# Performance work log

Hardware: AMD Instinct MI355X
Metric: run time of the kernel (lower is better)

The kernel has to match this reference:

```python
import jax, jax.numpy as jnp
import numpy as np
import math

B, N, L = 1, 256, 384
D_MSA, D_PAIR, H, DH = 256, 128, 8, 32
EPS = 1e-5


def layernorm(x, g, b):
    mu = jnp.mean(x, axis=-1, keepdims=True)
    var = jnp.mean(jnp.square(x - mu), axis=-1, keepdims=True)
    return (x - mu) * jax.lax.rsqrt(var + EPS) * g + b


def setup_inputs() -> dict:
    key = jax.random.key(0)
    ks = jax.random.split(key, 16)
    s_msa = 1.0 / math.sqrt(D_MSA)
    s_pair = 1.0 / math.sqrt(D_PAIR)
    s_hd = 1.0 / math.sqrt(H * DH)
    return {
        "msa": jax.random.normal(ks[0], (B, N, L, D_MSA), jnp.float32),
        "pair": jax.random.normal(ks[1], (B, L, L, D_PAIR), jnp.float32),
        "ln_msa_g": jnp.ones((D_MSA,), jnp.float32),
        "ln_msa_b": jnp.zeros((D_MSA,), jnp.float32),
        "ln_pair_g": jnp.ones((D_PAIR,), jnp.float32),
        "ln_pair_b": jnp.zeros((D_PAIR,), jnp.float32),
        # SequenceWeight projections (stored as (in, out): y = x @ W + b)
        "Wq_sw": jax.random.normal(ks[2], (D_MSA, H * DH), jnp.float32) * s_msa,
        "bq_sw": jnp.zeros((H * DH,), jnp.float32),
        "Wk_sw": jax.random.normal(ks[3], (D_MSA, H * DH), jnp.float32) * s_msa,
        "bk_sw": jnp.zeros((H * DH,), jnp.float32),
        # Main attention projections (bias-free q/k/v)
        "Wq": jax.random.normal(ks[4], (D_MSA, H * DH), jnp.float32) * s_msa,
        "Wk": jax.random.normal(ks[5], (D_MSA, H * DH), jnp.float32) * s_msa,
        "Wv": jax.random.normal(ks[6], (D_MSA, H * DH), jnp.float32) * s_msa,
        "Wb": jax.random.normal(ks[7], (D_PAIR, H), jnp.float32) * s_pair,
        "Wg": jax.random.normal(ks[8], (D_MSA, H * DH), jnp.float32) * s_msa,
        "bg": jnp.ones((H * DH,), jnp.float32),
        "Wo": jax.random.normal(ks[9], (H * DH, D_MSA), jnp.float32) * s_hd,
        "bo": jnp.zeros((D_MSA,), jnp.float32),
    }


def reference(msa, pair, ln_msa_g, ln_msa_b, ln_pair_g, ln_pair_b,
              Wq_sw, bq_sw, Wk_sw, bk_sw, Wq, Wk, Wv, Wb, Wg, bg, Wo, bo):
    b, n, l, _ = msa.shape
    scale = 1.0 / math.sqrt(DH)

    m = layernorm(msa, ln_msa_g, ln_msa_b)  # (B,N,L,d_msa)

    # --- SequenceWeight: per-sequence, per-position, per-head weights ---
    q_sw = (m[:, 0] @ Wq_sw + bq_sw).reshape(b, l, H, DH) * scale   # (B,L,h,d)
    k_sw = (m @ Wk_sw + bk_sw).reshape(b, n, l, H, DH)              # (B,N,L,h,d)
    sw_logits = jnp.einsum('bihd,bnihd->bnih', q_sw, k_sw)
    seq_weight = jax.nn.softmax(sw_logits, axis=1)[..., None]       # (B,N,L,h,1)

    # --- Row attention with pair bias ---
    q = (m @ Wq).reshape(b, n, l, H, DH) * seq_weight               # seq-weighted queries
    k = (m @ Wk).reshape(b, n, l, H, DH) * scale
    logits = jnp.einsum('bnihd,bnjhd->bijh', q, k)                  # sum over N and d
    bias = layernorm(pair, ln_pair_g, ln_pair_b) @ Wb               # (B,L,L,h)
    attn = jax.nn.softmax(logits + bias, axis=2)                    # softmax over j

    v = (m @ Wv).reshape(b, n, l, H, DH)
    out = jnp.einsum('bijh,bnjhd->bnihd', attn, v).reshape(b, n, l, H * DH)

    gate = jax.nn.sigmoid(m @ Wg + bg)
    return (out * gate) @ Wo + bo                                   # (B,N,L,d_msa)
```

## Files before the change

kernel.cpp:

```cpp
#include <hip/hip_runtime.h>
#include <stdint.h>

#define NSEQ 256
#define LRES 384
#define NH   8
#define NL   (NSEQ*LRES)
#define SCALE 0.17677669529663687f

typedef unsigned short u16;
typedef unsigned int   u32;
typedef short bf16x8 __attribute__((ext_vector_type(8)));
typedef float f32x4  __attribute__((ext_vector_type(4)));

__device__ __forceinline__ u16 f2bf(float f) {
    u32 x = __float_as_uint(f);
    return (u16)((x + 0x7fffu + ((x >> 16) & 1u)) >> 16);
}
__device__ __forceinline__ u32 pack2(float a, float b) {
    u32 xa = __float_as_uint(a);
    u32 xb = __float_as_uint(b);
    xa = (xa + 0x7fffu + ((xa >> 16) & 1u)) >> 16;
    xb = ((xb + 0x7fffu + ((xb >> 16) & 1u)) >> 16) << 16;
    return xa | xb;
}
__device__ __forceinline__ uint4 pack8(const float f[8]) {
    uint4 r;
    r.x = pack2(f[0], f[1]); r.y = pack2(f[2], f[3]);
    r.z = pack2(f[4], f[5]); r.w = pack2(f[6], f[7]);
    return r;
}
__device__ __forceinline__ void unpack2(u32 u, float& f0, float& f1) {
    f0 = __uint_as_float((u & 0xffffu) << 16);
    f1 = __uint_as_float(u & 0xffff0000u);
}
__device__ __forceinline__ void unpack8(uint4 p, float f[8]) {
    unpack2(p.x, f[0], f[1]);
    unpack2(p.y, f[2], f[3]);
    unpack2(p.z, f[4], f[5]);
    unpack2(p.w, f[6], f[7]);
}

__device__ __forceinline__ float wred_sum(float v) {
#pragma unroll
    for (int o = 32; o > 0; o >>= 1) v += __shfl_xor(v, o, 64);
    return v;
}
__device__ __forceinline__ float wred_max(float v) {
#pragma unroll
    for (int o = 32; o > 0; o >>= 1) v = fmaxf(v, __shfl_xor(v, o, 64));
    return v;
}

__global__ __launch_bounds__(256) void ln_msa_k(
    const float* __restrict__ x, const float* __restrict__ g,
    const float* __restrict__ b, u16* __restrict__ lnA,
    float* __restrict__ stats)
{
    const int lane = threadIdx.x & 63;
    const int row = blockIdx.x * 4 + (threadIdx.x >> 6);
    const size_t base = (size_t)row * 256 + lane * 4;
    float4 v = *(const float4*)(x + base);
    float s  = wred_sum(v.x + v.y + v.z + v.w);
    float sq = wred_sum(v.x*v.x + v.y*v.y + v.z*v.z + v.w*v.w);
    const float mu  = s * (1.f / 256.f);
    const float var = sq * (1.f / 256.f) - mu * mu;
    const float rs  = rsqrtf(var + 1e-5f);
    if (lane == 0) {
        stats[(size_t)row * 2]     = mu;
        stats[(size_t)row * 2 + 1] = rs;
    }
    float4 gg = *(const float4*)(g + lane * 4);
    float4 bb = *(const float4*)(b + lane * 4);
    float f0 = (v.x - mu) * rs * gg.x + bb.x;
    float f1 = (v.y - mu) * rs * gg.y + bb.y;
    float f2 = (v.z - mu) * rs * gg.z + bb.z;
    float f3 = (v.w - mu) * rs * gg.w + bb.w;
    uint2 pk;
    pk.x = pack2(f0, f1);
    pk.y = pack2(f2, f3);
    *(uint2*)(lnA + base) = pk;
}

__global__ __launch_bounds__(256) void wconv_k(
    const float* __restrict__ W0, const float* __restrict__ W1,
    const float* __restrict__ W2, const float* __restrict__ W3,
    const float* __restrict__ W4, const float* __restrict__ W5,
    u16* __restrict__ outAll)
{
    const float* Wsrc[6] = {W0, W1, W2, W3, W4, W5};
    const int widx = blockIdx.x >> 4;
    const int tile = blockIdx.x & 15;
    const int kt = tile >> 2, ct = tile & 3;
    const float* W = Wsrc[widx];
    __shared__ float ts[64][65];
    const int r  = threadIdx.x >> 2;
    const int cg = threadIdx.x & 3;
#pragma unroll
    for (int jj = 0; jj < 4; ++jj) {
        float4 v = *(const float4*)(W + (size_t)(kt * 64 + r) * 256
                                      + ct * 64 + cg * 16 + jj * 4);
        ts[r][cg * 16 + jj * 4 + 0] = v.x;
        ts[r][cg * 16 + jj * 4 + 1] = v.y;
        ts[r][cg * 16 + jj * 4 + 2] = v.z;
        ts[r][cg * 16 + jj * 4 + 3] = v.w;
    }
    __syncthreads();
    float lo[8], hi[8];
#pragma unroll
    for (int j = 0; j < 8; ++j) lo[j] = ts[cg * 16 + j][r];
#pragma unroll
    for (int j = 0; j < 8; ++j) hi[j] = ts[cg * 16 + 8 + j][r];
    u16* o = outAll + (size_t)widx * 65536 + (size_t)(ct * 64 + r) * 256
           + kt * 64 + cg * 16;
    *(uint4*)(o)     = pack8(lo);
    *(uint4*)(o + 8) = pack8(hi);
}

enum { MODE_QSW = 1 };

__global__ __launch_bounds__(256) void gemm_ln_k(
    const void* __restrict__ Av, int a_bf16,
    const float* __restrict__ stats,
    const float* __restrict__ lng, const float* __restrict__ lnb,
    const float* __restrict__ W, const float* __restrict__ bias,
    void* __restrict__ out, const float* __restrict__ seqw, int mode)
{
    __shared__ float As_t[32][68];
    __shared__ float Ws[32][132];
    __shared__ float gs[256], bs[256];
    const int tid = threadIdx.x;
    const int bx = blockIdx.y;
    const int by = blockIdx.x;
    const int tx = tid & 15, ty = tid >> 4;
    const int ar = tid >> 2, acg = tid & 3;
    const int wr = tid >> 3, wcg = tid & 7;
    const bool do_ln = (stats != nullptr);

    if (do_ln) { gs[tid] = lng[tid]; bs[tid] = lnb[tid]; }
    __syncthreads();

    const int arow_idx = by * 64 + ar;
    float mu = 0.f, rsg = 0.f;
    if (do_ln) {
        mu  = stats[(size_t)arow_idx * 2];
        rsg = stats[(size_t)arow_idx * 2 + 1];
    }

    float acc[4][8];
#pragma unroll
    for (int i = 0; i < 4; ++i)
#pragma unroll
        for (int j = 0; j < 8; ++j) acc[i][j] = 0.f;

    const size_t arow = (size_t)arow_idx * 256 + acg * 8;

    for (int kk = 0; kk < 256; kk += 32) {
        float af[8];
        if (a_bf16) {
            uint4 a8 = *(const uint4*)((const u16*)Av + arow + kk);
            unpack8(a8, af);
        } else {
            float4 x0 = *(const float4*)((const float*)Av + arow + kk);
            float4 x1 = *(const float4*)((const float*)Av + arow + kk + 4);
            af[0] = x0.x; af[1] = x0.y; af[2] = x0.z; af[3] = x0.w;
            af[4] = x1.x; af[5] = x1.y; af[6] = x1.z; af[7] = x1.w;
        }
        const float* wrow = W + (size_t)(kk + wr) * 256 + bx * 128 + wcg * 16;
        float4 w0 = *(const float4*)(wrow);
        float4 w1 = *(const float4*)(wrow + 4);
        float4 w2 = *(const float4*)(wrow + 8);
        float4 w3 = *(const float4*)(wrow + 12);
        if (do_ln) {
#pragma unroll
            for (int j = 0; j < 8; ++j) {
                const int k = kk + acg * 8 + j;
                af[j] = (af[j] - mu) * rsg * gs[k] + bs[k];
            }
        }
        __syncthreads();
#pragma unroll
        for (int j = 0; j < 8; ++j) As_t[acg * 8 + j][ar] = af[j];
        float* wsrow = &Ws[wr][wcg * 16];
        *(float4*)(wsrow)      = w0;
        *(float4*)(wsrow + 4)  = w1;
        *(float4*)(wsrow + 8)  = w2;
        *(float4*)(wsrow + 12) = w3;
        __syncthreads();
#pragma unroll 8
        for (int k = 0; k < 32; ++k) {
            const float4 a  = *(const float4*)&As_t[k][ty * 4];
            const float4 b0 = *(const float4*)&Ws[k][tx * 8];
            const float4 b1 = *(const float4*)&Ws[k][tx * 8 + 4];
            const float av[4] = {a.x, a.y, a.z, a.w};
            const float bv[8] = {b0.x, b0.y, b0.z, b0.w, b1.x, b1.y, b1.z, b1.w};
#pragma unroll
            for (int i = 0; i < 4; ++i)
#pragma unroll
                for (int j = 0; j < 8; ++j)
                    acc[i][j] = fmaf(av[i], bv[j], acc[i][j]);
        }
    }

    const int gc0 = bx * 128 + tx * 8;
    float bias8[8] = {0.f, 0.f, 0.f, 0.f, 0.f, 0.f, 0.f, 0.f};
    if (bias) {
#pragma unroll
        for (int j = 0; j < 8; ++j) bias8[j] = bias[gc0 + j];
    }

    float* o = (float*)out;
#pragma unroll
    for (int i = 0; i < 4; ++i) {
        const size_t gr = (size_t)by * 64 + ty * 4 + i;
#pragma unroll
        for (int j = 0; j < 8; ++j)
            o[gr * 256 + gc0 + j] = (acc[i][j] + bias8[j]) * SCALE;
    }
}

__global__ __launch_bounds__(256) void swl_dot_k(
    const float* __restrict__ qsw, const u16* __restrict__ ksw,
    float* __restrict__ swl)
{
    const int gid = blockIdx.x * 256 + threadIdx.x;
    const int r = gid >> 3, h = gid & 7;
    const int i = r % LRES;
    const float* qp = qsw + (size_t)i * 256 + h * 32;
    const uint4* kp = (const uint4*)(ksw + (size_t)r * 256 + h * 32);
    float s = 0.f;
#pragma unroll
    for (int g4 = 0; g4 < 4; ++g4) {
        float kf[8]; unpack8(kp[g4], kf);
#pragma unroll
        for (int j = 0; j < 8; ++j) s += qp[g4 * 8 + j] * kf[j];
    }
    swl[gid] = s;
}

__global__ __launch_bounds__(256) void softmax_n_k(float* __restrict__ swl)
{
    const int col = blockIdx.x * 4 + (threadIdx.x >> 6);
    const int lane = threadIdx.x & 63;
    float* base = swl + col;
    float v[4];
#pragma unroll
    for (int t = 0; t < 4; ++t) v[t] = base[(size_t)(lane * 4 + t) * 3072];
    float mx = wred_max(fmaxf(fmaxf(v[0], v[1]), fmaxf(v[2], v[3])));
    float e[4], s = 0.f;
#pragma unroll
    for (int t = 0; t < 4; ++t) { e[t] = __expf(v[t] - mx); s += e[t]; }
    s = wred_sum(s);
    const float inv = 1.f / s;
#pragma unroll
    for (int t = 0; t < 4; ++t) base[(size_t)(lane * 4 + t) * 3072] = e[t] * inv;
}

__global__ __launch_bounds__(256) void pair_bias_k(
    const float* __restrict__ pair, const float* __restrict__ g,
    const float* __restrict__ b, const float* __restrict__ Wb,
    float* __restrict__ biasH)
{
    const int lane = threadIdx.x & 63;
    const size_t rp = (size_t)blockIdx.x * 4 + (threadIdx.x >> 6);
    float2 u = *(const float2*)(pair + rp * 128 + lane * 2);
    float f0 = u.x, f1 = u.y;
    float s  = wred_sum(f0 + f1);
    float sq = wred_sum(f0 * f0 + f1 * f1);
    float mu  = s * (1.f / 128.f);
    float var = sq * (1.f / 128.f) - mu * mu;
    float rs  = rsqrtf(var + 1e-5f);
    const int c0 = lane * 2;
    float xn0 = (f0 - mu) * rs * g[c0]     + b[c0];
    float xn1 = (f1 - mu) * rs * g[c0 + 1] + b[c0 + 1];
    float4 wa0 = *(const float4*)(Wb + (size_t)c0 * 8);
    float4 wa1 = *(const float4*)(Wb + (size_t)c0 * 8 + 4);
    float4 wb0 = *(const float4*)(Wb + (size_t)(c0 + 1) * 8);
    float4 wb1 = *(const float4*)(Wb + (size_t)(c0 + 1) * 8 + 4);
    const float wa[8] = {wa0.x, wa0.y, wa0.z, wa0.w, wa1.x, wa1.y, wa1.z, wa1.w};
    const float wb_[8] = {wb0.x, wb0.y, wb0.z, wb0.w, wb1.x, wb1.y, wb1.z, wb1.w};
    float acc[8];
#pragma unroll
    for (int h = 0; h < 8; ++h) acc[h] = wred_sum(xn0 * wa[h] + xn1 * wb_[h]);
    if (lane == 0) {
#pragma unroll
        for (int h = 0; h < 8; ++h) biasH[rp * 8 + h] = acc[h];
    }
}

__device__ __forceinline__ void stage128x64(
    const u16* __restrict__ src, size_t rowStride, u16* lds, int tid)
{
    const int row   = tid >> 1;
    const int cbase = (tid & 1) * 4;
#pragma unroll
    for (int ch = 0; ch < 4; ++ch) {
        const int cc = cbase + ch;
        const uint4 v = *(const uint4*)(src + (size_t)row * rowStride + cc * 8);
        *(uint4*)(lds + row * 64 + ((cc ^ (row & 7)) * 8)) = v;
    }
}

__device__ __forceinline__ bf16x8 frag_read(const u16* lds, int row, int kchunk)
{
    return *(const bf16x8*)(lds + row * 64 + ((kchunk ^ (row & 7)) * 8));
}

enum { PROJ_KSW = 0, PROJ_QT = 1, PROJ_KT = 2, PROJ_VT = 3,
       PROJ_GATE = 4, PROJ_OUT = 5 };

__global__ __launch_bounds__(256) void proj_mfma(
    const u16* __restrict__ A, const u16* __restrict__ Wt,
    const float* __restrict__ bias, const float* __restrict__ seqw,
    void* __restrict__ out, int mode)
{
    __shared__ u16 tA[128 * 64];
    __shared__ u16 tW[128 * 64];

    int wg = (blockIdx.x & 7) * 192 + (blockIdx.x >> 3);
    const int rowTile = wg >> 1;
    const int colTile = wg & 1;

    const int tid  = threadIdx.x;
    const int lane = tid & 63, wid = tid >> 6;
    const int wr = wid >> 1, wc = wid & 1;
    const int g  = lane >> 4;
    const int mrow = wr * 64 + (lane & 15);
    const int nrow = wc * 64 + (lane & 15);

    f32x4 acc[4][4];
#pragma unroll
    for (int m = 0; m < 4; ++m)
#pragma unroll
        for (int n = 0; n < 4; ++n) {
            f32x4 z = {0.f, 0.f, 0.f, 0.f};
            acc[m][n] = z;
        }

    const u16* Ab = A  + (size_t)rowTile * 128 * 256;
    const u16* Wb = Wt + (size_t)colTile * 128 * 256;

    for (int k0 = 0; k0 < 256; k0 += 64) {
        stage128x64(Ab + k0, 256, tA, tid);
        stage128x64(Wb + k0, 256, tW, tid);
        __syncthreads();
#pragma unroll
        for (int ks = 0; ks < 2; ++ks) {
            bf16x8 wf[4], af[4];
#pragma unroll
            for (int m = 0; m < 4; ++m) wf[m] = frag_read(tW, mrow + m * 16, ks * 4 + g);
#pragma unroll
            for (int n = 0; n < 4; ++n) af[n] = frag_read(tA, nrow + n * 16, ks * 4 + g);
#pragma unroll
            for (int m = 0; m < 4; ++m)
#pragma unroll
                for (int n = 0; n < 4; ++n)
                    acc[m][n] = __builtin_amdgcn_mfma_f32_16x16x32_bf16(
                        wf[m], af[n], acc[m][n], 0, 0, 0);
        }
        __syncthreads();
    }

    const int cq0 = colTile * 128 + wr * 64 + ((lane >> 4) << 2);
    const int r0  = rowTile * 128 + wc * 64 + (lane & 15);

#pragma unroll
    for (int m = 0; m < 4; ++m) {
        const int c = cq0 + m * 16;
#pragma unroll
        for (int n = 0; n < 4; ++n) {
            const int r = r0 + n * 16;
            const f32x4 a = acc[m][n];
            if (mode == PROJ_KSW || mode == PROJ_GATE) {
                float f0 = a[0] + bias[c];
                float f1 = a[1] + bias[c + 1];
                float f2 = a[2] + bias[c + 2];
                float f3 = a[3] + bias[c + 3];
                if (mode == PROJ_GATE) {
                    f0 = 1.f / (1.f + __expf(-f0));
                    f1 = 1.f / (1.f + __expf(-f1));
                    f2 = 1.f / (1.f + __expf(-f2));
                    f3 = 1.f / (1.f + __expf(-f3));
                }
                uint2 pk;
                pk.x = pack2(f0, f1);
                pk.y = pack2(f2, f3);
                *(uint2*)((u16*)out + (size_t)r * 256 + c) = pk;
            } else if (mode == PROJ_QT || mode == PROJ_KT) {
                const int h = c >> 5, d = c & 31;
                const int n_ = r / LRES, ii = r % LRES;
                const float mult = (mode == PROJ_QT)
                    ? seqw[(size_t)r * NH + h] : SCALE;
                uint2 pk;
                pk.x = pack2(a[0] * mult, a[1] * mult);
                pk.y = pack2(a[2] * mult, a[3] * mult);
                *(uint2*)((u16*)out + (size_t)h * 3145728
                          + (size_t)ii * 8192 + n_ * 32 + d) = pk;
            } else if (mode == PROJ_VT) {
                const int h = c >> 5, d = c & 31;
                const int n_ = r / LRES, ii = r % LRES;
                u16* o = (u16*)out + (size_t)h * 3145728
                       + (size_t)(n_ * 32 + d) * 384 + ii;
                o[0]   = f2bf(a[0]);
                o[384] = f2bf(a[1]);
                o[768] = f2bf(a[2]);
                o[1152] = f2bf(a[3]);
            } else {
                float* o = (float*)out + (size_t)r * 256 + c;
                o[0] = a[0] + bias[c];
                o[1] = a[1] + bias[c + 1];
                o[2] = a[2] + bias[c + 2];
                o[3] = a[3] + bias[c + 3];
            }
        }
    }
}

__global__ __launch_bounds__(256) void gemm_logits_mfma(
    const u16* __restrict__ qT, const u16* __restrict__ kT,
    float* __restrict__ part)
{
    __shared__ u16 tQ[128 * 64];
    __shared__ u16 tK[128 * 64];

    int wg = (blockIdx.x & 7) * 36 + (blockIdx.x >> 3);
    const int gsel = wg / 9;
    const int t    = wg % 9;
    const int h  = gsel >> 2, kc = gsel & 3;
    const int bi = t / 3, bj = t % 3;

    const u16* Q = qT + (size_t)h * 3145728 + (size_t)bi * 128 * 8192;
    const u16* K = kT + (size_t)h * 3145728 + (size_t)bj * 128 * 8192;

    const int tid  = threadIdx.x;
    const int lane = tid & 63, wid = tid >> 6;
    const int wr = wid >> 1, wc = wid & 1;
    const int g  = lane >> 4;
    const int mrow = wr * 64 + (lane & 15);
    const int nrow = wc * 64 + (lane & 15);

    f32x4 acc[4][4];
#pragma unroll
    for (int m = 0; m < 4; ++m)
#pragma unroll
        for (int n = 0; n < 4; ++n) {
            f32x4 z = {0.f, 0.f, 0.f, 0.f};
            acc[m][n] = z;
        }

    const int k0beg = kc * 2048, k0end = k0beg + 2048;
    for (int k0 = k0beg; k0 < k0end; k0 += 64) {
        stage128x64(Q + k0, 8192, tQ, tid);
        stage128x64(K + k0, 8192, tK, tid);
        __syncthreads();
#pragma unroll
        for (int ks = 0; ks < 2; ++ks) {
            bf16x8 kf[4], qf[4];
#pragma unroll
            for (int m = 0; m < 4; ++m) kf[m] = frag_read(tK, mrow + m * 16, ks * 4 + g);
#pragma unroll
            for (int n = 0; n < 4; ++n) qf[n] = frag_read(tQ, nrow + n * 16, ks * 4 + g);
#pragma unroll
            for (int m = 0; m < 4; ++m)
#pragma unroll
                for (int n = 0; n < 4; ++n)
                    acc[m][n] = __builtin_amdgcn_mfma_f32_16x16x32_bf16(
                        kf[m], qf[n], acc[m][n], 0, 0, 0);
        }
        __syncthreads();
    }

    float* dst = part + (size_t)kc * 1179648 + (size_t)h * 147456;
    const int gj_base = bj * 128 + wr * 64 + ((lane >> 4) << 2);
    const int gi_base = bi * 128 + wc * 64 + (lane & 15);
#pragma unroll
    for (int m = 0; m < 4; ++m)
#pragma unroll
        for (int n = 0; n < 4; ++n) {
            const int gi = gi_base + n * 16;
            const int gj = gj_base + m * 16;
            *(f32x4*)(dst + (size_t)gi * 384 + gj) = acc[m][n];
        }
}

__global__ __launch_bounds__(256) void softmax_j_k(
    const float* __restrict__ part, const float* __restrict__ biasH,
    u16* __restrict__ attnB)
{
    const int row = blockIdx.x * 4 + (threadIdx.x >> 6);
    const int lane = threadIdx.x & 63;
    const int h = row / LRES, i = row % LRES;
    const float* p = part + (size_t)h * 147456 + (size_t)i * 384;
    const float* bh = biasH + (size_t)i * 3072 + h;
    float v[6];
#pragma unroll
    for (int t = 0; t < 6; ++t) {
        const int j = t * 64 + lane;
        v[t] = p[j] + p[j + 1179648] + p[j + 2359296] + p[j + 3538944]
             + bh[(size_t)j * 8];
    }
    float mx = v[0];
#pragma unroll
    for (int t = 1; t < 6; ++t) mx = fmaxf(mx, v[t]);
    mx = wred_max(mx);
    float e[6], s = 0.f;
#pragma unroll
    for (int t = 0; t < 6; ++t) { e[t] = __expf(v[t] - mx); s += e[t]; }
    s = wred_sum(s);
    const float inv = 1.f / s;
    u16* ab = attnB + (size_t)h * 147456 + (size_t)i * 384;
#pragma unroll
    for (int t = 0; t < 6; ++t) ab[t * 64 + lane] = f2bf(e[t] * inv);
}

__global__ __launch_bounds__(256) void gemm_out_mfma(
    const u16* __restrict__ attnB, const u16* __restrict__ vTT,
    u16* gate_io)
{
    __shared__ u16 tV[128 * 64];
    __shared__ u16 tA[128 * 64];

    int wg = (blockIdx.x & 7) * 192 + (blockIdx.x >> 3);
    const int h  = wg / 192;
    const int r  = wg % 192;
    const int bn = r / 3;
    const int bi = r % 3;

    const u16* A = attnB + (size_t)h * 147456 + (size_t)bi * 128 * 384;
    const u16* V = vTT   + (size_t)h * 3145728 + (size_t)bn * 128 * 384;

    const int tid  = threadIdx.x;
    const int lane = tid & 63, wid = tid >> 6;
    const int wr = wid >> 1, wc = wid & 1;
    const int g  = lane >> 4;
    const int mrow = wr * 64 + (lane & 15);
    const int nrow = wc * 64 + (lane & 15);

    f32x4 acc[4][4];
#pragma unroll
    for (int m = 0; m < 4; ++m)
#pragma unroll
        for (int n = 0; n < 4; ++n) {
            f32x4 z = {0.f, 0.f, 0.f, 0.f};
            acc[m][n] = z;
        }

    for (int j0 = 0; j0 < 384; j0 += 64) {
        stage128x64(V + j0, 384, tV, tid);
        stage128x64(A + j0, 384, tA, tid);
        __syncthreads();
#pragma unroll
        for (int ks = 0; ks < 2; ++ks) {
            bf16x8 vf[4], af[4];
#pragma unroll
            for (int m = 0; m < 4; ++m) vf[m] = frag_read(tV, mrow + m * 16, ks * 4 + g);
#pragma unroll
            for (int n = 0; n < 4; ++n) af[n] = frag_read(tA, nrow + n * 16, ks * 4 + g);
#pragma unroll
            for (int m = 0; m < 4; ++m)
#pragma unroll
                for (int n = 0; n < 4; ++n)
                    acc[m][n] = __builtin_amdgcn_mfma_f32_16x16x32_bf16(
                        vf[m], af[n], acc[m][n], 0, 0, 0);
        }
        __syncthreads();
    }

    const int nd_base = bn * 128 + wr * 64 + ((lane >> 4) << 2);
    const int i_base  = bi * 128 + wc * 64 + (lane & 15);
#pragma unroll
    for (int m = 0; m < 4; ++m) {
        const int nd = nd_base + m * 16;
        const int nseq = nd >> 5, d = nd & 31;
#pragma unroll
        for (int n = 0; n < 4; ++n) {
            const int gi = i_base + n * 16;
            const size_t addr = ((size_t)(nseq * LRES + gi)) * 256 + h * 32 + d;
            uint2 g2 = *(const uint2*)(gate_io + addr);
            float gf[4];
            unpack2(g2.x, gf[0], gf[1]);
            unpack2(g2.y, gf[2], gf[3]);
            const f32x4 a = acc[m][n];
            uint2 pk;
            pk.x = pack2(a[0] * gf[0], a[1] * gf[1]);
            pk.y = pack2(a[2] * gf[2], a[3] * gf[3]);
            *(uint2*)(gate_io + addr) = pk;
        }
    }
}

extern "C" void kernel_launch(void* const* d_in, const int* in_sizes, int n_in,
                              void* d_out, int out_size, void* d_ws, size_t ws_size,
                              hipStream_t stream)
{
    const float* msa       = (const float*)d_in[0];
    const float* pair      = (const float*)d_in[1];
    const float* ln_msa_g  = (const float*)d_in[2];
    const float* ln_msa_b  = (const float*)d_in[3];
    const float* ln_pair_g = (const float*)d_in[4];
    const float* ln_pair_b = (const float*)d_in[5];
    const float* Wq_sw     = (const float*)d_in[6];
    const float* bq_sw     = (const float*)d_in[7];
    const float* Wk_sw     = (const float*)d_in[8];
    const float* bk_sw     = (const float*)d_in[9];
    const float* Wq        = (const float*)d_in[10];
    const float* Wk        = (const float*)d_in[11];
    const float* Wv        = (const float*)d_in[12];
    const float* Wb        = (const float*)d_in[13];
    const float* Wg        = (const float*)d_in[14];
    const float* bg        = (const float*)d_in[15];
    const float* Wo        = (const float*)d_in[16];
    const float* bo        = (const float*)d_in[17];
    float* out = (float*)d_out;

    char* ws = (char*)d_ws;
    u16*   slotA  = (u16*)(ws + 0);
    u16*   slotB  = (u16*)(ws + 50331648);
    float* stats  = (float*)(ws + 100663296);
    float* qsw    = (float*)(ws + 101449728);
    float* swl    = (float*)(ws + 101842944);
    float* biasH  = (float*)(ws + 104988672);
    float* part   = (float*)(ws + 109707264);
    u16*   attnB  = (u16*)(ws + 128581632);
    u16*   lnA    = (u16*)(ws + 130940928);
    u16*   WtAll  = (u16*)(ws + 181272576);

    u16* Wt_ksw = WtAll;
    u16* Wt_q   = WtAll + 65536;
    u16* Wt_k   = WtAll + 131072;
    u16* Wt_v   = WtAll + 196608;
    u16* Wt_g   = WtAll + 262144;
    u16* Wt_o   = WtAll + 327680;

    ln_msa_k<<<NL / 4, 256, 0, stream>>>(msa, ln_msa_g, ln_msa_b, lnA, stats);
    wconv_k<<<96, 256, 0, stream>>>(Wk_sw, Wq, Wk, Wv, Wg, Wo, WtAll);
    proj_mfma<<<1536, 256, 0, stream>>>(lnA, Wt_ksw, bk_sw, nullptr, slotA, PROJ_KSW);
    gemm_ln_k<<<dim3(LRES / 64, 2), 256, 0, stream>>>(
        msa, 0, stats, ln_msa_g, ln_msa_b, Wq_sw, bq_sw, qsw, nullptr, MODE_QSW);
    swl_dot_k<<<NL * NH / 256, 256, 0, stream>>>(qsw, slotA, swl);
    softmax_n_k<<<LRES * NH / 4, 256, 0, stream>>>(swl);
    proj_mfma<<<1536, 256, 0, stream>>>(lnA, Wt_q, nullptr, swl, slotA, PROJ_QT);
    proj_mfma<<<1536, 256, 0, stream>>>(lnA, Wt_k, nullptr, nullptr, slotB, PROJ_KT);
    pair_bias_k<<<LRES * LRES / 4, 256, 0, stream>>>(
        pair, ln_pair_g, ln_pair_b, Wb, biasH);
    gemm_logits_mfma<<<288, 256, 0, stream>>>(slotA, slotB, part);
    softmax_j_k<<<NH * LRES / 4, 256, 0, stream>>>(part, biasH, attnB);
    proj_mfma<<<1536, 256, 0, stream>>>(lnA, Wt_v, nullptr, nullptr, slotA, PROJ_VT);
    proj_mfma<<<1536, 256, 0, stream>>>(lnA, Wt_g, bg, nullptr, slotB, PROJ_GATE);
    gemm_out_mfma<<<1536, 256, 0, stream>>>(attnB, slotA, slotB);
    proj_mfma<<<1536, 256, 0, stream>>>(slotB, Wt_o, bo, nullptr, out, PROJ_OUT);
}
```

Before: 700.4 us.

## Fold pair LayerNorm affine into Wb and process 8 pair rows per wave

A tiny prep kernel precomputes Wb scaled by the LN gain plus the per-head column sums of the scaled weights and of the bias-weighted weights. This lets the pair-bias kernel apply the normalization after the projection as rs*(x·W') - rs*mu*A + B. The pair-bias kernel now gives each row 8 lanes with 16 channels each, so one wave covers 8 rows. It replaces many full-wave reductions with in-register dot products and a 3-step butterfly shuffle, cutting shuffle and reduction overhead on a memory-bound pass over the 75MB pair tensor. It adds one extra small kernel launch.

After: 640.2 us. 1.09x faster.

```diff
diff --git a/kernel.cpp b/kernel.cpp
--- a/kernel.cpp
+++ b/kernel.cpp
@@ -114,6 +114,40 @@
            + kt * 64 + cg * 16;
     *(uint4*)(o)     = pack8(lo);
     *(uint4*)(o + 8) = pack8(hi);
+}
+
+__global__ __launch_bounds__(128) void wbprep_k(
+    const float* __restrict__ g, const float* __restrict__ b,
+    const float* __restrict__ Wb, float* __restrict__ Wp,
+    float* __restrict__ AB)
+{
+    __shared__ float ps[128][8];
+    __shared__ float pb[128][8];
+    const int c = threadIdx.x;
+    const float gc = g[c], bc = b[c];
+    float4 w0 = *(const float4*)(Wb + (size_t)c * 8);
+    float4 w1 = *(const float4*)(Wb + (size_t)c * 8 + 4);
+    const float wraw[8] = {w0.x, w0.y, w0.z, w0.w, w1.x, w1.y, w1.z, w1.w};
+    float wp[8];
+#pragma unroll
+    for (int h = 0; h < 8; ++h) {
+        wp[h] = wraw[h] * gc;
+        ps[c][h] = wp[h];
+        pb[c][h] = wraw[h] * bc;
+    }
+    *(float4*)(Wp + (size_t)c * 8)     = make_float4(wp[0], wp[1], wp[2], wp[3]);
+    *(float4*)(Wp + (size_t)c * 8 + 4) = make_float4(wp[4], wp[5], wp[6], wp[7]);
+    __syncthreads();
+    if (c < 8) {
+        float a = 0.f;
+        for (int j = 0; j < 128; ++j) a += ps[j][c];
+        AB[c] = a;
+    } else if (c < 16) {
+        const int h = c - 8;
+        float a = 0.f;
+        for (int j = 0; j < 128; ++j) a += pb[j][h];
+        AB[8 + h] = a;
+    }
 }
 
 enum { MODE_QSW = 1 };
@@ -256,35 +290,63 @@
 }
 
 __global__ __launch_bounds__(256) void pair_bias_k(
-    const float* __restrict__ pair, const float* __restrict__ g,
-    const float* __restrict__ b, const float* __restrict__ Wb,
-    float* __restrict__ biasH)
-{
-    const int lane = threadIdx.x & 63;
-    const size_t rp = (size_t)blockIdx.x * 4 + (threadIdx.x >> 6);
-    float2 u = *(const float2*)(pair + rp * 128 + lane * 2);
-    float f0 = u.x, f1 = u.y;
-    float s  = wred_sum(f0 + f1);
-    float sq = wred_sum(f0 * f0 + f1 * f1);
-    float mu  = s * (1.f / 128.f);
-    float var = sq * (1.f / 128.f) - mu * mu;
-    float rs  = rsqrtf(var + 1e-5f);
-    const int c0 = lane * 2;
-    float xn0 = (f0 - mu) * rs * g[c0]     + b[c0];
-    float xn1 = (f1 - mu) * rs * g[c0 + 1] + b[c0 + 1];
-    float4 wa0 = *(const float4*)(Wb + (size_t)c0 * 8);
-    float4 wa1 = *(const float4*)(Wb + (size_t)c0 * 8 + 4);
-    float4 wb0 = *(const float4*)(Wb + (size_t)(c0 + 1) * 8);
-    float4 wb1 = *(const float4*)(Wb + (size_t)(c0 + 1) * 8 + 4);
-    const float wa[8] = {wa0.x, wa0.y, wa0.z, wa0.w, wa1.x, wa1.y, wa1.z, wa1.w};
-    const float wb_[8] = {wb0.x, wb0.y, wb0.z, wb0.w, wb1.x, wb1.y, wb1.z, wb1.w};
+    const float* __restrict__ pairX, const float* __restrict__ Wp,
+    const float* __restrict__ AB, float* __restrict__ biasH)
+{
+    __shared__ float ws[128][8];
+    __shared__ float As[8], Bs[8];
+    const int tid = threadIdx.x;
+    {
+        float4 w4 = *(const float4*)(Wp + tid * 4);
+        *(float4*)(&ws[tid >> 1][(tid & 1) * 4]) = w4;
+    }
+    if (tid < 8)       As[tid] = AB[tid];
+    else if (tid < 16) Bs[tid - 8] = AB[tid];
+    __syncthreads();
+
+    const int lane = tid & 63;
+    const int p  = lane >> 3;
+    const int cg = lane & 7;
+    const size_t pb = (size_t)blockIdx.x * 32 + (tid >> 6) * 8 + p;
+    const float* src = pairX + pb * 128 + cg * 16;
+    float x[16];
+    *(float4*)(x)      = *(const float4*)(src);
+    *(float4*)(x + 4)  = *(const float4*)(src + 4);
+    *(float4*)(x + 8)  = *(const float4*)(src + 8);
+    *(float4*)(x + 12) = *(const float4*)(src + 12);
+
+    float s = 0.f, sq = 0.f;
+#pragma unroll
+    for (int j = 0; j < 16; ++j) { s += x[j]; sq += x[j] * x[j]; }
+#pragma unroll
+    for (int o = 1; o <= 4; o <<= 1) {
+        s  += __shfl_xor(s, o, 64);
+        sq += __shfl_xor(sq, o, 64);
+    }
+    const float mu  = s * (1.f / 128.f);
+    const float var = sq * (1.f / 128.f) - mu * mu;
+    const float rs  = rsqrtf(var + 1e-5f);
+
     float acc[8];
 #pragma unroll
-    for (int h = 0; h < 8; ++h) acc[h] = wred_sum(xn0 * wa[h] + xn1 * wb_[h]);
-    if (lane == 0) {
-#pragma unroll
-        for (int h = 0; h < 8; ++h) biasH[rp * 8 + h] = acc[h];
-    }
+    for (int hh = 0; hh < 8; ++hh) {
+        const int h = hh ^ cg;
+        float a = 0.f;
+#pragma unroll
+        for (int j = 0; j < 16; ++j) a += x[j] * ws[cg * 16 + j][h];
+        acc[hh] = a;
+    }
+#pragma unroll
+    for (int o = 1; o <= 4; o <<= 1) {
+        float nv[8];
+#pragma unroll
+        for (int hh = 0; hh < 8; ++hh)
+            nv[hh] = acc[hh] + __shfl_xor(acc[hh ^ o], o, 64);
+#pragma unroll
+        for (int hh = 0; hh < 8; ++hh) acc[hh] = nv[hh];
+    }
+    const float res = rs * acc[0] - rs * mu * As[cg] + Bs[cg];
+    biasH[pb * 8 + cg] = res;
 }
 
 __device__ __forceinline__ void stage128x64(
@@ -623,6 +685,8 @@
     u16*   attnB  = (u16*)(ws + 128581632);
     u16*   lnA    = (u16*)(ws + 130940928);
     u16*   WtAll  = (u16*)(ws + 181272576);
+    float* Wp     = (float*)(ws + 182059008);
+    float* AB     = (float*)(ws + 182063104);
 
     u16* Wt_ksw = WtAll;
     u16* Wt_q   = WtAll + 65536;
@@ -633,6 +697,7 @@
 
     ln_msa_k<<<NL / 4, 256, 0, stream>>>(msa, ln_msa_g, ln_msa_b, lnA, stats);
     wconv_k<<<96, 256, 0, stream>>>(Wk_sw, Wq, Wk, Wv, Wg, Wo, WtAll);
+    wbprep_k<<<1, 128, 0, stream>>>(ln_pair_g, ln_pair_b, Wb, Wp, AB);
     proj_mfma<<<1536, 256, 0, stream>>>(lnA, Wt_ksw, bk_sw, nullptr, slotA, PROJ_KSW);
     gemm_ln_k<<<dim3(LRES / 64, 2), 256, 0, stream>>>(
         msa, 0, stats, ln_msa_g, ln_msa_b, Wq_sw, bq_sw, qsw, nullptr, MODE_QSW);
@@ -640,8 +705,7 @@
     softmax_n_k<<<LRES * NH / 4, 256, 0, stream>>>(swl);
     proj_mfma<<<1536, 256, 0, stream>>>(lnA, Wt_q, nullptr, swl, slotA, PROJ_QT);
     proj_mfma<<<1536, 256, 0, stream>>>(lnA, Wt_k, nullptr, nullptr, slotB, PROJ_KT);
-    pair_bias_k<<<LRES * LRES / 4, 256, 0, stream>>>(
-        pair, ln_pair_g, ln_pair_b, Wb, biasH);
+    pair_bias_k<<<LRES * LRES / 32, 256, 0, stream>>>(pair, Wp, AB, biasH);
     gemm_logits_mfma<<<288, 256, 0, stream>>>(slotA, slotB, part);
     softmax_j_k<<<NH * LRES / 4, 256, 0, stream>>>(part, biasH, attnB);
     proj_mfma<<<1536, 256, 0, stream>>>(lnA, Wt_v, nullptr, nullptr, slotA, PROJ_VT);
```
